# Kernel tuning notes

Measured on AMD Instinct MI355X. Metric: run time of the kernel, lower is better.

Reference implementation:

```python
import jax, jax.numpy as jnp
import numpy as np

ALPHA = 0.2  # LeakyReLU negative slope


def setup_inputs() -> dict:
    key = jax.random.key(0)
    k_h, k_adj, k_a1, k_a2 = jax.random.split(key, 4)
    B, N, D = 8, 2048, 128
    h = jax.random.normal(k_h, (B, N, D), dtype=jnp.float32)
    adj = jax.random.randint(k_adj, (B, N, N), 0, 2, dtype=jnp.int32)
    # attention parameters a1, a2: shape (D, 1) as in the original layer
    a1 = jax.random.normal(k_a1, (D, 1), dtype=jnp.float32) * (1.0 / np.sqrt(D))
    a2 = jax.random.normal(k_a2, (D, 1), dtype=jnp.float32) * (1.0 / np.sqrt(D))
    return {"h": h, "adj": adj, "a1": a1, "a2": a2}


def reference(h, adj, a1, a2):
    # h: [B, N, D]; adj: [B, N, N] (int mask); a1, a2: [D, 1]
    f1 = h @ a1                                  # [B, N, 1] per-source score
    f2 = h @ a2                                  # [B, N, 1] per-target score
    logits = f1 + jnp.swapaxes(f2, 1, 2)         # broadcast -> [B, N, N]
    logits = jnp.where(logits > 0, logits, ALPHA * logits)  # LeakyReLU
    logits = jnp.where(adj > 0, logits, -jnp.inf)            # adjacency mask
    prob = jax.nn.softmax(logits, axis=2)        # [B, N, N]
    h_prime = jnp.einsum('bij,bjd->bid', prob, h)  # weighted aggregation
    return jax.nn.elu(h_prime)                   # concat=True branch
```

## Files before the change

### kernel.cpp

```cpp
#include <hip/hip_runtime.h>
#include <hip/hip_bf16.h>
#include <math.h>

#define BB 8
#define NN 2048
#define DD 128
#define ALPHA 0.2f
#define LOG2E 1.4426950408889634f

typedef __attribute__((ext_vector_type(8))) short short8;
typedef __attribute__((ext_vector_type(4))) float f32x4;

__device__ inline unsigned short bf16_rne(float v) {
    unsigned int x = __float_as_uint(v);
    unsigned int r = x + 0x7FFFu + ((x >> 16) & 1u);
    return (unsigned short)(r >> 16);
}

__global__ __launch_bounds__(256) void bitpack_kernel(const int* __restrict__ adj,
                                                      unsigned* __restrict__ bits) {
    unsigned g0 = blockIdx.x * 256 + threadIdx.x;
#pragma unroll
    for (int rep = 0; rep < 2; ++rep) {
        unsigned g = g0 + rep * 524288u;
        const int4* p = reinterpret_cast<const int4*>(adj + (size_t)g * 32);
        int4 v[8];
#pragma unroll
        for (int i = 0; i < 8; ++i) v[i] = p[i];
        unsigned w = 0;
#pragma unroll
        for (int i = 0; i < 8; ++i) {
            w |= ((unsigned)v[i].x) << (4 * i);
            w |= ((unsigned)v[i].y) << (4 * i + 1);
            w |= ((unsigned)v[i].z) << (4 * i + 2);
            w |= ((unsigned)v[i].w) << (4 * i + 3);
        }
        bits[g] = w;
    }
}

__global__ __launch_bounds__(256) void pack_kernel(const float* __restrict__ h,
                                                   const float* __restrict__ a1,
                                                   const float* __restrict__ a2,
                                                   float* __restrict__ f1,
                                                   float* __restrict__ f2,
                                                   unsigned short* __restrict__ panel) {
    __shared__ float hs[32][DD];
    int blk = blockIdx.x;
    int b   = blk >> 6;
    int ks  = blk & 63;
    int r0  = ks * 32;
    int t   = threadIdx.x;

    const float* hb = h + ((size_t)b * NN + r0) * DD;
#pragma unroll
    for (int m = 0; m < 4; ++m) {
        int off = t * 4 + m * 1024;
        *reinterpret_cast<float4*>(&hs[0][0] + off) =
            *reinterpret_cast<const float4*>(hb + off);
    }
    __syncthreads();

    {
        int row = t >> 3, d0 = (t & 7) * 16;
        float s1 = 0.f, s2 = 0.f;
#pragma unroll
        for (int q = 0; q < 4; ++q) {
            float4 hv  = *reinterpret_cast<const float4*>(&hs[row][d0 + q * 4]);
            float4 av1 = *reinterpret_cast<const float4*>(a1 + d0 + q * 4);
            float4 av2 = *reinterpret_cast<const float4*>(a2 + d0 + q * 4);
            s1 += hv.x * av1.x + hv.y * av1.y + hv.z * av1.z + hv.w * av1.w;
            s2 += hv.x * av2.x + hv.y * av2.y + hv.z * av2.z + hv.w * av2.w;
        }
#pragma unroll
        for (int off = 1; off < 8; off <<= 1) {
            s1 += __shfl_xor(s1, off, 64);
            s2 += __shfl_xor(s2, off, 64);
        }
        if ((t & 7) == 0) {
            f1[b * NN + r0 + row] = s1 * LOG2E;
            f2[b * NN + r0 + row] = s2 * LOG2E;
        }
    }

    {
        int n = t >> 1;
        size_t base = (((size_t)b * 64 + ks) * 128 + n) * 32;
#pragma unroll
        for (int cc = 0; cc < 2; ++cc) {
            int c = (t & 1) * 2 + cc;
            short8 v;
#pragma unroll
            for (int e = 0; e < 8; ++e) v[e] = (short)bf16_rne(hs[c * 8 + e][n]);
            *reinterpret_cast<short8*>(panel + base + (size_t)c * 8) = v;
        }
    }
}

__global__ __launch_bounds__(256, 3) void gat_mfma(const unsigned* __restrict__ bits,
                                                   const float* __restrict__ f1,
                                                   const float* __restrict__ f2,
                                                   const unsigned short* __restrict__ panel,
                                                   float* __restrict__ out) {
    __shared__ float buf[2][16][132];
    __shared__ float sden[4][16];

    int blk  = blockIdx.x;
    int b    = blk & 7;
    int tile = blk >> 3;
    int i0   = tile * 16;
    int t    = threadIdx.x;
    int w    = t >> 6, l = t & 63;
    int lr   = l & 15, lc = l >> 4;

    const unsigned short* pb = panel + (size_t)b * (64 * 128 * 32);
    const float* f2b = f2 + b * NN;
    float f1r = f1[b * NN + i0 + lr];

    int kbase = w * 512;
    const unsigned* brow = bits + (((size_t)(b * NN + i0 + lr)) << 6) + (kbase >> 5);

    f32x4 acc[8];
#pragma unroll
    for (int nt = 0; nt < 8; ++nt) acc[nt] = (f32x4){0.f, 0.f, 0.f, 0.f};
    f32x4 accd = (f32x4){0.f, 0.f, 0.f, 0.f};

    short8 ones;
#pragma unroll
    for (int e = 0; e < 8; ++e) ones[e] = (short)0x3F80;

    unsigned bcur = brow[0];
    float4 g0c = *reinterpret_cast<const float4*>(f2b + kbase + lc * 8);
    float4 g1c = *reinterpret_cast<const float4*>(f2b + kbase + lc * 8 + 4);

#pragma unroll 2
    for (int ks = 0; ks < 16; ++ks) {
        int k0 = kbase + ks * 32;
        unsigned bs = bcur >> (lc * 8);
        float4 g0 = g0c, g1 = g1c;

        const unsigned short* pk = pb + (size_t)(k0 >> 5) * 4096 + lr * 32 + lc * 8;
        short8 bf[8];
#pragma unroll
        for (int nt = 0; nt < 8; ++nt)
            bf[nt] = *reinterpret_cast<const short8*>(pk + nt * 512);

        if (ks < 15) {
            bcur = brow[ks + 1];
            int jn = k0 + 32 + lc * 8;
            g0c = *reinterpret_cast<const float4*>(f2b + jn);
            g1c = *reinterpret_cast<const float4*>(f2b + jn + 4);
        }

        float f2v[8] = {g0.x, g0.y, g0.z, g0.w, g1.x, g1.y, g1.z, g1.w};
        float wv[8];
#pragma unroll
        for (int e = 0; e < 8; ++e) {
            float x  = f1r + f2v[e];
            float ee = fmaxf(x, ALPHA * x);
            float gv = __builtin_amdgcn_exp2f(ee);
            wv[e] = ((bs >> e) & 1u) ? gv : 0.f;
        }
        union { short8 s; __hip_bfloat162 h2[4]; } u;
#pragma unroll
        for (int p = 0; p < 4; ++p)
            u.h2[p] = __float22bfloat162_rn(make_float2(wv[2 * p], wv[2 * p + 1]));

#pragma unroll
        for (int nt = 0; nt < 8; ++nt)
            acc[nt] = __builtin_amdgcn_mfma_f32_16x16x32_bf16(u.s, bf[nt], acc[nt], 0, 0, 0);
        accd = __builtin_amdgcn_mfma_f32_16x16x32_bf16(u.s, ones, accd, 0, 0, 0);
    }

    if ((l & 15) == 0) {
#pragma unroll
        for (int r = 0; r < 4; ++r) sden[w][(l >> 4) * 4 + r] = accd[r];
    }

    float* mybuf = &buf[w >> 1][0][0];
    if ((w & 1) == 0) {
#pragma unroll
        for (int nt = 0; nt < 8; ++nt) {
            float* p = mybuf + (lc * 4) * 132 + nt * 16 + lr;
#pragma unroll
            for (int r = 0; r < 4; ++r) p[r * 132] = acc[nt][r];
        }
    }
    __syncthreads();
    if (w & 1) {
#pragma unroll
        for (int nt = 0; nt < 8; ++nt) {
            float* p = mybuf + (lc * 4) * 132 + nt * 16 + lr;
#pragma unroll
            for (int r = 0; r < 4; ++r) p[r * 132] += acc[nt][r];
        }
    }
    __syncthreads();

    {
        int row = t >> 4, col0 = (t & 15) * 8;
        float den = sden[0][row] + sden[1][row] + sden[2][row] + sden[3][row];
        float inv = 1.0f / den;
        float* ob = out + ((size_t)b * NN + i0 + row) * DD;
#pragma unroll
        for (int q = 0; q < 2; ++q) {
            int col = col0 + q * 4;
            float4 v0 = *reinterpret_cast<const float4*>(&buf[0][row][col]);
            float4 v1 = *reinterpret_cast<const float4*>(&buf[1][row][col]);
            float r0 = (v0.x + v1.x) * inv;
            float r1 = (v0.y + v1.y) * inv;
            float r2 = (v0.z + v1.z) * inv;
            float r3 = (v0.w + v1.w) * inv;
            r0 = (r0 > 0.f) ? r0 : expm1f(r0);
            r1 = (r1 > 0.f) ? r1 : expm1f(r1);
            r2 = (r2 > 0.f) ? r2 : expm1f(r2);
            r3 = (r3 > 0.f) ? r3 : expm1f(r3);
            *reinterpret_cast<float4*>(ob + col) = make_float4(r0, r1, r2, r3);
        }
    }
}

extern "C" void kernel_launch(void* const* d_in, const int* in_sizes, int n_in,
                              void* d_out, int out_size, void* d_ws, size_t ws_size,
                              hipStream_t stream) {
    const float* h   = (const float*)d_in[0];
    const int*   adj = (const int*)d_in[1];
    const float* a1  = (const float*)d_in[2];
    const float* a2  = (const float*)d_in[3];
    float* out = (float*)d_out;

    float* f1 = (float*)d_ws;
    float* f2 = f1 + BB * NN;
    unsigned short* panel = (unsigned short*)(f2 + BB * NN);
    unsigned* bits = (unsigned*)(panel + (size_t)BB * 64 * 128 * 32);

    bitpack_kernel<<<2048, 256, 0, stream>>>(adj, bits);
    pack_kernel<<<BB * 64, 256, 0, stream>>>(h, a1, a2, f1, f2, panel);
    gat_mfma<<<BB * 128, 256, 0, stream>>>(bits, f1, f2, panel, out);
}
```

Baseline: 250.4 us.

## Share panel tiles across 64-row blocks via double-buffered LDS staging

Each aggregation block now covers 64 output rows with 8 waves: four row tiles, each split across two K halves. The bf16 h panel is copied into LDS through a double-buffered `global_load_lds` pipeline, so one panel load serves four row tiles instead of each wave fetching its own fragments from global memory. This cuts repeated L2/global traffic on the panel. In exchange the grid shrinks to 256 blocks of 512 threads, the main loop gains a barrier on every step, and LDS use rises. There is also a risk that the async LDS loads are not waited on before the buffers are read.

Result: faster. 241.4 us (-3.6%).

```diff
diff --git a/kernel.cpp b/kernel.cpp
--- a/kernel.cpp
+++ b/kernel.cpp
@@ -15,6 +15,12 @@
     unsigned int x = __float_as_uint(v);
     unsigned int r = x + 0x7FFFu + ((x >> 16) & 1u);
     return (unsigned short)(r >> 16);
+}
+
+__device__ __forceinline__ void stage16(const void* gsrc, void* lds) {
+    __builtin_amdgcn_global_load_lds(
+        (const __attribute__((address_space(1))) unsigned int*)gsrc,
+        (__attribute__((address_space(3))) unsigned int*)lds, 16, 0, 0);
 }
 
 __global__ __launch_bounds__(256) void bitpack_kernel(const int* __restrict__ adj,
@@ -97,28 +103,29 @@
     }
 }
 
-__global__ __launch_bounds__(256, 3) void gat_mfma(const unsigned* __restrict__ bits,
+__global__ __launch_bounds__(512, 2) void gat_mfma(const unsigned* __restrict__ bits,
                                                    const float* __restrict__ f1,
                                                    const float* __restrict__ f2,
                                                    const unsigned short* __restrict__ panel,
                                                    float* __restrict__ out) {
-    __shared__ float buf[2][16][132];
-    __shared__ float sden[4][16];
+    __shared__ __align__(16) unsigned char stg[2][16384];
+    __shared__ __align__(16) float red[4][16][132];
+    __shared__ float sden[4][2][16];
 
     int blk  = blockIdx.x;
     int b    = blk & 7;
     int tile = blk >> 3;
-    int i0   = tile * 16;
+    int i0   = tile * 64;
     int t    = threadIdx.x;
     int w    = t >> 6, l = t & 63;
     int lr   = l & 15, lc = l >> 4;
-
-    const unsigned short* pb = panel + (size_t)b * (64 * 128 * 32);
+    int mt   = w >> 1, kh = w & 1;
+
+    const unsigned char* pslice = (const unsigned char*)(panel + (size_t)b * (64 * 128 * 32));
     const float* f2b = f2 + b * NN;
-    float f1r = f1[b * NN + i0 + lr];
-
-    int kbase = w * 512;
-    const unsigned* brow = bits + (((size_t)(b * NN + i0 + lr)) << 6) + (kbase >> 5);
+    int irow = i0 + mt * 16 + lr;
+    float f1r = f1[b * NN + irow];
+    const unsigned* brow = bits + ((size_t)(b * NN + irow) << 6);
 
     f32x4 acc[8];
 #pragma unroll
@@ -129,27 +136,38 @@
 #pragma unroll
     for (int e = 0; e < 8; ++e) ones[e] = (short)0x3F80;
 
-    unsigned bcur = brow[0];
-    float4 g0c = *reinterpret_cast<const float4*>(f2b + kbase + lc * 8);
-    float4 g1c = *reinterpret_cast<const float4*>(f2b + kbase + lc * 8 + 4);
+    int soff = w * 1024 + l * 16;
+    int doff = w * 1024;
+
+    stage16(pslice + soff, stg[0] + doff);
+    stage16(pslice + 8192 + soff, stg[0] + 8192 + doff);
+
+    unsigned bcur = brow[kh];
+    float4 g0c = *reinterpret_cast<const float4*>(f2b + kh * 32 + lc * 8);
+    float4 g1c = *reinterpret_cast<const float4*>(f2b + kh * 32 + lc * 8 + 4);
+
+    const unsigned char* myfrag0 = &stg[0][0] + kh * 8192 + lr * 64 + lc * 16;
+    const unsigned char* myfrag1 = &stg[1][0] + kh * 8192 + lr * 64 + lc * 16;
 
 #pragma unroll 2
-    for (int ks = 0; ks < 16; ++ks) {
-        int k0 = kbase + ks * 32;
+    for (int s = 0; s < 32; ++s) {
+        int cur = s & 1;
+        __syncthreads();
+
+        if (s < 31) {
+            const unsigned char* src = pslice + (size_t)(s + 1) * 16384;
+            unsigned char* dst = stg[cur ^ 1];
+            stage16(src + soff, dst + doff);
+            stage16(src + 8192 + soff, dst + 8192 + doff);
+        }
+
         unsigned bs = bcur >> (lc * 8);
         float4 g0 = g0c, g1 = g1c;
-
-        const unsigned short* pk = pb + (size_t)(k0 >> 5) * 4096 + lr * 32 + lc * 8;
-        short8 bf[8];
-#pragma unroll
-        for (int nt = 0; nt < 8; ++nt)
-            bf[nt] = *reinterpret_cast<const short8*>(pk + nt * 512);
-
-        if (ks < 15) {
-            bcur = brow[ks + 1];
-            int jn = k0 + 32 + lc * 8;
-            g0c = *reinterpret_cast<const float4*>(f2b + jn);
-            g1c = *reinterpret_cast<const float4*>(f2b + jn + 4);
+        if (s < 31) {
+            int cn = 2 * (s + 1) + kh;
+            bcur = brow[cn];
+            g0c = *reinterpret_cast<const float4*>(f2b + cn * 32 + lc * 8);
+            g1c = *reinterpret_cast<const float4*>(f2b + cn * 32 + lc * 8 + 4);
         }
 
         float f2v[8] = {g0.x, g0.y, g0.z, g0.w, g1.x, g1.y, g1.z, g1.w};
@@ -161,36 +179,38 @@
             float gv = __builtin_amdgcn_exp2f(ee);
             wv[e] = ((bs >> e) & 1u) ? gv : 0.f;
         }
-        union { short8 s; __hip_bfloat162 h2[4]; } u;
+        union { short8 s8; __hip_bfloat162 h2[4]; } u;
 #pragma unroll
         for (int p = 0; p < 4; ++p)
             u.h2[p] = __float22bfloat162_rn(make_float2(wv[2 * p], wv[2 * p + 1]));
 
-#pragma unroll
-        for (int nt = 0; nt < 8; ++nt)
-            acc[nt] = __builtin_amdgcn_mfma_f32_16x16x32_bf16(u.s, bf[nt], acc[nt], 0, 0, 0);
-        accd = __builtin_amdgcn_mfma_f32_16x16x32_bf16(u.s, ones, accd, 0, 0, 0);
-    }
-
-    if ((l & 15) == 0) {
-#pragma unroll
-        for (int r = 0; r < 4; ++r) sden[w][(l >> 4) * 4 + r] = accd[r];
-    }
-
-    float* mybuf = &buf[w >> 1][0][0];
-    if ((w & 1) == 0) {
+        const unsigned char* frag = cur ? myfrag1 : myfrag0;
 #pragma unroll
         for (int nt = 0; nt < 8; ++nt) {
-            float* p = mybuf + (lc * 4) * 132 + nt * 16 + lr;
+            short8 bfv = *reinterpret_cast<const short8*>(frag + nt * 1024);
+            acc[nt] = __builtin_amdgcn_mfma_f32_16x16x32_bf16(u.s8, bfv, acc[nt], 0, 0, 0);
+        }
+        accd = __builtin_amdgcn_mfma_f32_16x16x32_bf16(u.s8, ones, accd, 0, 0, 0);
+    }
+
+    if (lr == 0) {
+#pragma unroll
+        for (int r = 0; r < 4; ++r) sden[mt][kh][lc * 4 + r] = accd[r];
+    }
+
+    if (kh == 0) {
+#pragma unroll
+        for (int nt = 0; nt < 8; ++nt) {
+            float* p = &red[mt][lc * 4][nt * 16 + lr];
 #pragma unroll
             for (int r = 0; r < 4; ++r) p[r * 132] = acc[nt][r];
         }
     }
     __syncthreads();
-    if (w & 1) {
+    if (kh == 1) {
 #pragma unroll
         for (int nt = 0; nt < 8; ++nt) {
-            float* p = mybuf + (lc * 4) * 132 + nt * 16 + lr;
+            float* p = &red[mt][lc * 4][nt * 16 + lr];
 #pragma unroll
             for (int r = 0; r < 4; ++r) p[r * 132] += acc[nt][r];
         }
@@ -198,19 +218,16 @@
     __syncthreads();
 
     {
-        int row = t >> 4, col0 = (t & 15) * 8;
-        float den = sden[0][row] + sden[1][row] + sden[2][row] + sden[3][row];
+        int row = t >> 3, col0 = (t & 7) * 16;
+        int rmt = row >> 4, rloc = row & 15;
+        float den = sden[rmt][0][rloc] + sden[rmt][1][rloc];
         float inv = 1.0f / den;
         float* ob = out + ((size_t)b * NN + i0 + row) * DD;
 #pragma unroll
-        for (int q = 0; q < 2; ++q) {
+        for (int q = 0; q < 4; ++q) {
             int col = col0 + q * 4;
-            float4 v0 = *reinterpret_cast<const float4*>(&buf[0][row][col]);
-            float4 v1 = *reinterpret_cast<const float4*>(&buf[1][row][col]);
-            float r0 = (v0.x + v1.x) * inv;
-            float r1 = (v0.y + v1.y) * inv;
-            float r2 = (v0.z + v1.z) * inv;
-            float r3 = (v0.w + v1.w) * inv;
+            float4 v = *reinterpret_cast<const float4*>(&red[rmt][rloc][col]);
+            float r0 = v.x * inv, r1 = v.y * inv, r2 = v.z * inv, r3 = v.w * inv;
             r0 = (r0 > 0.f) ? r0 : expm1f(r0);
             r1 = (r1 > 0.f) ? r1 : expm1f(r1);
             r2 = (r2 > 0.f) ? r2 : expm1f(r2);
@@ -236,5 +253,5 @@
 
     bitpack_kernel<<<2048, 256, 0, stream>>>(adj, bits);
     pack_kernel<<<BB * 64, 256, 0, stream>>>(h, a1, a2, f1, f2, panel);
-    gat_mfma<<<BB * 128, 256, 0, stream>>>(bits, f1, f2, panel, out);
-}
+    gat_mfma<<<BB * 32, 512, 0, stream>>>(bits, f1, f2, panel, out);
+}
```
